# Kernel tuning notes

Measured on AMD Instinct MI355X. Metric: run time of the kernel, lower is better.

## Reference

```python
import jax, jax.numpy as jnp
import numpy as np

B, N, C, H = 2, 2048, 512, 8
D = C // H  # head dim = 64
SCALE = C ** -0.5  # module uses heads_channels**-0.5 (full inner dim, not per-head)


def setup_inputs() -> dict:
    key = jax.random.key(0)
    ks = jax.random.split(key, 9)
    return {
        "q": jax.random.normal(ks[0], (B, N, C), jnp.float32),
        "kv": jax.random.normal(ks[1], (B, N, C), jnp.float32),
        "pos_q": jax.random.normal(ks[2], (B, N, D), jnp.float32),
        "pos_k": jax.random.normal(ks[3], (B, N, D), jnp.float32),
        "Wq": jax.random.normal(ks[4], (C, C), jnp.float32) * (C ** -0.5),
        "Wk": jax.random.normal(ks[5], (C, C), jnp.float32) * (C ** -0.5),
        "Wv": jax.random.normal(ks[6], (C, C), jnp.float32) * (C ** -0.5),
        "Wo": jax.random.normal(ks[7], (C, C), jnp.float32) * (C ** -0.5),
        "bo": jnp.zeros((C,), jnp.float32),
    }


def reference(q, kv, pos_q, pos_k, Wq, Wk, Wv, Wo, bo):
    # projections: [b n c] @ [c c] -> [b n c]
    qp = q @ Wq
    kp = kv @ Wk
    vp = kv @ Wv
    # split heads: b n (h d) -> b h n d
    split = lambda t: t.reshape(B, N, H, D).transpose(0, 2, 1, 3)
    qh, kh, vh = split(qp), split(kp), split(vp)
    # additive positional bias, broadcast over heads: b n d -> b 1 n d
    qh = qh + pos_q[:, None, :, :]
    kh = kh + pos_k[:, None, :, :]
    sim = jnp.einsum("bhid,bhjd->bhij", qh, kh) * SCALE
    attn = jax.nn.softmax(sim, axis=-1)
    out = jnp.einsum("bhij,bhjd->bhid", attn, vh)
    # merge heads: b h n d -> b n (h d)
    out = out.transpose(0, 2, 1, 3).reshape(B, N, C)
    return out @ Wo + bo
```

## Files before the change

### kernel.cpp

```cpp
#include <hip/hip_runtime.h>
#include <hip/hip_bf16.h>
#include <stdint.h>
#include <math.h>

static constexpr int kB = 2, kN = 2048, kC = 512, kH = 8, kD = 64;
static constexpr float kScaleL2E =
    (float)(0.044194173824159216 * 1.4426950408889634);
static constexpr float kShift = 12.0f;
static constexpr int kSplit = 2;
static constexpr size_t kSegF = (size_t)kB * kN * kC;

typedef short bf16x8 __attribute__((ext_vector_type(8)));
typedef short bf16x4 __attribute__((ext_vector_type(4)));
typedef float f32x4  __attribute__((ext_vector_type(4)));

__device__ __forceinline__ float bf2f(unsigned short u) {
  union { unsigned int i; float f; } v; v.i = ((unsigned int)u) << 16; return v.f;
}
__device__ __forceinline__ unsigned short f2bf(float f) {
  union { float f; unsigned int i; } v; v.f = f;
  unsigned int x = v.i;
  return (unsigned short)((x + 0x7FFFu + ((x >> 16) & 1u)) >> 16);
}
__device__ __forceinline__ short f2bs(float f) { return (short)f2bf(f); }
__device__ __forceinline__ unsigned int pack2_t(float lo, float hi) {
  union { float f; unsigned int i; } a, b; a.f = lo; b.f = hi;
  return (b.i & 0xFFFF0000u) | (a.i >> 16);
}

__device__ __forceinline__ int vcol(int k) {
  return 32 * (k >> 5) + ((k >> 2) & 3) * 8 + ((k >> 4) & 1) * 4;
}

__global__ __launch_bounds__(256) void prep_kernel(
    const float* __restrict__ q, const float* __restrict__ kv,
    const float* __restrict__ Wq, const float* __restrict__ Wk,
    const float* __restrict__ Wv,
    unsigned short* __restrict__ qbf, unsigned short* __restrict__ kvbf,
    unsigned short* __restrict__ wT)
{
  const int t = threadIdx.x;
  if (blockIdx.z == 0) {
    const int gid = blockIdx.x * 256 + t;
    #pragma unroll
    for (int it = 0; it < 8; ++it) {
      int i4 = gid + it * 65536;
      float4 a = *(const float4*)(q + (size_t)i4 * 4);
      float4 b = *(const float4*)(kv + (size_t)i4 * 4);
      bf16x4 ab = {f2bs(a.x), f2bs(a.y), f2bs(a.z), f2bs(a.w)};
      bf16x4 bb = {f2bs(b.x), f2bs(b.y), f2bs(b.z), f2bs(b.w)};
      *(bf16x4*)(qbf + (size_t)i4 * 4) = ab;
      *(bf16x4*)(kvbf + (size_t)i4 * 4) = bb;
    }
  } else {
    if (blockIdx.x >= 192) return;
    const int wsel = blockIdx.x >> 6;
    const int tile = blockIdx.x & 63;
    const int tr = tile >> 3, tc = tile & 7;
    const float* W = (wsel == 0) ? Wq : (wsel == 1 ? Wk : Wv);
    unsigned short* out = wT + (size_t)wsel * kC * kC;

    __shared__ __align__(16) float Ts[64][68];
    #pragma unroll
    for (int it = 0; it < 4; ++it) {
      int e = t + it * 256;
      int r = e >> 4, c4 = (e & 15) * 4;
      *(float4*)&Ts[r][c4] =
          *(const float4*)(W + (size_t)(tr * 64 + r) * kC + tc * 64 + c4);
    }
    __syncthreads();
    const int n = t >> 2, ks = (t & 3) * 16;
    unsigned short* orow = out + (size_t)(tc * 64 + n) * kC + tr * 64 + ks;
    #pragma unroll
    for (int c = 0; c < 4; ++c) {
      ushort4 o;
      o.x = f2bf(Ts[ks + c * 4 + 0][n]);
      o.y = f2bf(Ts[ks + c * 4 + 1][n]);
      o.z = f2bf(Ts[ks + c * 4 + 2][n]);
      o.w = f2bf(Ts[ks + c * 4 + 3][n]);
      *(ushort4*)(orow + c * 4) = o;
    }
  }
}

__global__ __launch_bounds__(256) void proj_kernel(
    const unsigned short* __restrict__ qbf,
    const unsigned short* __restrict__ kvbf,
    const unsigned short* __restrict__ wT,
    const float* __restrict__ pos_q,
    const float* __restrict__ pos_k,
    unsigned short* __restrict__ qh,
    unsigned short* __restrict__ kh,
    unsigned short* __restrict__ vhT)
{
  const bool kvmode = (blockIdx.z == 1);
  const unsigned short* A = kvmode ? kvbf : qbf;
  const unsigned short* Bt0 = wT + (kvmode ? (size_t)kC * kC : 0);
  const unsigned short* Bt1 = wT + 2 * (size_t)kC * kC;

  __shared__ __align__(16) unsigned short As[128][72];
  __shared__ __align__(16) unsigned short Bs[2][64][72];

  const int t = threadIdx.x;
  const int w = t >> 6, lane = t & 63;
  const int l15 = lane & 15, quad = lane >> 4;
  const int m0 = blockIdx.x * 128;
  const int n0 = blockIdx.y * 64;

  const int sr = t >> 3, sc = (t & 7) * 8;

  bf16x8 pa[4], pb0[2], pb1[2];
  #pragma unroll
  for (int i = 0; i < 4; ++i)
    pa[i] = *(const bf16x8*)(A + (size_t)(m0 + sr + i * 32) * kC + sc);
  #pragma unroll
  for (int i = 0; i < 2; ++i)
    pb0[i] = *(const bf16x8*)(Bt0 + (size_t)(n0 + sr + i * 32) * kC + sc);
  if (kvmode)
    #pragma unroll
    for (int i = 0; i < 2; ++i)
      pb1[i] = *(const bf16x8*)(Bt1 + (size_t)(n0 + sr + i * 32) * kC + sc);

  f32x4 acc0[2][4], acc1[2][4];
  #pragma unroll
  for (int si = 0; si < 2; ++si)
    #pragma unroll
    for (int ct = 0; ct < 4; ++ct) {
      acc0[si][ct] = (f32x4){0.f, 0.f, 0.f, 0.f};
      acc1[si][ct] = (f32x4){0.f, 0.f, 0.f, 0.f};
    }

  for (int k0 = 0; k0 < kC; k0 += 64) {
    if (k0) __syncthreads();
    #pragma unroll
    for (int i = 0; i < 4; ++i) *(bf16x8*)&As[sr + i * 32][sc] = pa[i];
    #pragma unroll
    for (int i = 0; i < 2; ++i) *(bf16x8*)&Bs[0][sr + i * 32][sc] = pb0[i];
    if (kvmode)
      #pragma unroll
      for (int i = 0; i < 2; ++i) *(bf16x8*)&Bs[1][sr + i * 32][sc] = pb1[i];
    __syncthreads();
    if (k0 + 64 < kC) {
      int kn = k0 + 64;
      #pragma unroll
      for (int i = 0; i < 4; ++i)
        pa[i] = *(const bf16x8*)(A + (size_t)(m0 + sr + i * 32) * kC + kn + sc);
      #pragma unroll
      for (int i = 0; i < 2; ++i)
        pb0[i] = *(const bf16x8*)(Bt0 + (size_t)(n0 + sr + i * 32) * kC + kn + sc);
      if (kvmode)
        #pragma unroll
        for (int i = 0; i < 2; ++i)
          pb1[i] = *(const bf16x8*)(Bt1 + (size_t)(n0 + sr + i * 32) * kC + kn + sc);
    }
    bf16x8 a0[2], a1[2];
    #pragma unroll
    for (int si = 0; si < 2; ++si) {
      a0[si] = *(const bf16x8*)&As[w * 32 + si * 16 + l15][quad * 8];
      a1[si] = *(const bf16x8*)&As[w * 32 + si * 16 + l15][32 + quad * 8];
    }
    #pragma unroll
    for (int ct = 0; ct < 4; ++ct) {
      bf16x8 b0 = *(const bf16x8*)&Bs[0][ct * 16 + l15][quad * 8];
      bf16x8 b1 = *(const bf16x8*)&Bs[0][ct * 16 + l15][32 + quad * 8];
      #pragma unroll
      for (int si = 0; si < 2; ++si) {
        acc0[si][ct] = __builtin_amdgcn_mfma_f32_16x16x32_bf16(a0[si], b0, acc0[si][ct], 0, 0, 0);
        acc0[si][ct] = __builtin_amdgcn_mfma_f32_16x16x32_bf16(a1[si], b1, acc0[si][ct], 0, 0, 0);
      }
      if (kvmode) {
        bf16x8 c0 = *(const bf16x8*)&Bs[1][ct * 16 + l15][quad * 8];
        bf16x8 c1 = *(const bf16x8*)&Bs[1][ct * 16 + l15][32 + quad * 8];
        #pragma unroll
        for (int si = 0; si < 2; ++si) {
          acc1[si][ct] = __builtin_amdgcn_mfma_f32_16x16x32_bf16(a0[si], c0, acc1[si][ct], 0, 0, 0);
          acc1[si][ct] = __builtin_amdgcn_mfma_f32_16x16x32_bf16(a1[si], c1, acc1[si][ct], 0, 0, 0);
        }
      }
    }
  }

  const int h = n0 >> 6;
  if (!kvmode) {
    #pragma unroll
    for (int si = 0; si < 2; ++si)
      #pragma unroll
      for (int r = 0; r < 4; ++r) {
        int m = m0 + w * 32 + si * 16 + quad * 4 + r;
        int b = m >> 11, n_seq = m & (kN - 1);
        #pragma unroll
        for (int ct = 0; ct < 4; ++ct) {
          int d = ct * 16 + l15;
          float val = (acc0[si][ct][r] +
                       pos_q[((size_t)b * kN + n_seq) * kD + d]) * kScaleL2E;
          qh[(((size_t)b * kH + h) * kN + n_seq) * kD + d] = f2bf(val);
        }
      }
  } else {
    #pragma unroll
    for (int si = 0; si < 2; ++si)
      #pragma unroll
      for (int r = 0; r < 4; ++r) {
        int m = m0 + w * 32 + si * 16 + quad * 4 + r;
        int b = m >> 11, n_seq = m & (kN - 1);
        #pragma unroll
        for (int ct = 0; ct < 4; ++ct) {
          int d = ct * 16 + l15;
          float vk = acc0[si][ct][r] + pos_k[((size_t)b * kN + n_seq) * kD + d];
          kh[(((size_t)b * kH + h) * kN + n_seq) * kD + d] = f2bf(vk);
        }
      }
    __syncthreads();
    unsigned short (*Tv)[136] = (unsigned short(*)[136])&As[0][0];
    #pragma unroll
    for (int si = 0; si < 2; ++si)
      #pragma unroll
      for (int ct = 0; ct < 4; ++ct) {
        const int d = ct * 16 + l15;
        const int nl = w * 32 + si * 16 + quad * 4;
        unsigned int lo = (unsigned int)f2bf(acc1[si][ct][0]) |
                          ((unsigned int)f2bf(acc1[si][ct][1]) << 16);
        unsigned int hi = (unsigned int)f2bf(acc1[si][ct][2]) |
                          ((unsigned int)f2bf(acc1[si][ct][3]) << 16);
        *(unsigned int*)&Tv[d][nl]     = lo;
        *(unsigned int*)&Tv[d][nl + 2] = hi;
      }
    __syncthreads();
    const int c16 = t & 15, dr = t >> 4;
    const int b2 = m0 >> 11, nbase = m0 & (kN - 1);
    #pragma unroll
    for (int rep = 0; rep < 4; ++rep) {
      const int d = rep * 16 + dr;
      bf16x8 vv = *(const bf16x8*)&Tv[d][c16 * 8];
      *(bf16x8*)(vhT + (((size_t)(b2 * kH + h)) * kD + d) * kN + nbase + c16 * 8) = vv;
    }
  }
}

__global__ __launch_bounds__(256, 8) void attn_kernel(
    const unsigned short* __restrict__ qh,
    const unsigned short* __restrict__ kh,
    const unsigned short* __restrict__ vhT,
    unsigned short* __restrict__ opart,
    float* __restrict__ lbuf)
{
  const int sid = (blockIdx.x & 7) * 128 + (blockIdx.x >> 3);
  const int s  = sid >> 9;
  const int bh = (sid >> 5) & 15;
  const int q0 = (sid & 31) * 64;
  const int b = bh >> 3, h = bh & 7;
  const int kbase = s * (kN / kSplit);
  const int nkt = kN / kSplit / 64;
  const int t = threadIdx.x;
  const int w = t >> 6, lane = t & 63;
  const int l15 = lane & 15, quad = lane >> 4;

  __shared__ __align__(16) unsigned short Kb_s[64][72];
  __shared__ __align__(16) unsigned short Vt_s[64][72];

  const unsigned short* Qb = qh  + (size_t)bh * kN * kD;
  const unsigned short* Kb = kh  + (size_t)bh * kN * kD;
  const unsigned short* Vb = vhT + (size_t)bh * kD * kN;

  bf16x8 aq0, aq1;
  {
    const unsigned short* qrow = Qb + (size_t)(q0 + w * 16 + l15) * kD;
    aq0 = *(const bf16x8*)(qrow + quad * 8);
    aq1 = *(const bf16x8*)(qrow + 32 + quad * 8);
  }

  const int sr = t >> 3, sc = (t & 7) * 8, sr2 = sr + 32;
  const int vc1 = vcol(sc), vc2 = vcol(sc + 4);

  bf16x8 pk0 = *(const bf16x8*)(Kb + (size_t)(kbase + sr) * kD + sc);
  bf16x8 pk1 = *(const bf16x8*)(Kb + (size_t)(kbase + sr2) * kD + sc);
  bf16x8 pv0 = *(const bf16x8*)(Vb + (size_t)sr * kN + kbase + sc);
  bf16x8 pv1 = *(const bf16x8*)(Vb + (size_t)sr2 * kN + kbase + sc);

  f32x4 o[4];
  #pragma unroll
  for (int nt = 0; nt < 4; ++nt) o[nt] = (f32x4){0.f, 0.f, 0.f, 0.f};
  float l_run = 0.f;

  for (int i = 0; i < nkt; ++i) {
    __syncthreads();
    *(bf16x8*)&Kb_s[sr][sc]  = pk0;
    *(bf16x8*)&Kb_s[sr2][sc] = pk1;
    {
      bf16x4 lo0 = {pv0[0], pv0[1], pv0[2], pv0[3]};
      bf16x4 hi0 = {pv0[4], pv0[5], pv0[6], pv0[7]};
      bf16x4 lo1 = {pv1[0], pv1[1], pv1[2], pv1[3]};
      bf16x4 hi1 = {pv1[4], pv1[5], pv1[6], pv1[7]};
      *(bf16x4*)&Vt_s[sr][vc1]  = lo0;
      *(bf16x4*)&Vt_s[sr][vc2]  = hi0;
      *(bf16x4*)&Vt_s[sr2][vc1] = lo1;
      *(bf16x4*)&Vt_s[sr2][vc2] = hi1;
    }
    __syncthreads();

    f32x4 sacc[4];
    __builtin_amdgcn_s_setprio(1);
    #pragma unroll
    for (int ct = 0; ct < 4; ++ct) {
      bf16x8 ak0 = *(const bf16x8*)&Kb_s[ct * 16 + l15][quad * 8];
      bf16x8 ak1 = *(const bf16x8*)&Kb_s[ct * 16 + l15][32 + quad * 8];
      f32x4 zz = (f32x4){0.f, 0.f, 0.f, 0.f};
      zz = __builtin_amdgcn_mfma_f32_16x16x32_bf16(ak0, aq0, zz, 0, 0, 0);
      zz = __builtin_amdgcn_mfma_f32_16x16x32_bf16(ak1, aq1, zz, 0, 0, 0);
      sacc[ct] = zz;
    }
    __builtin_amdgcn_s_setprio(0);

    if (i + 1 < nkt) {
      int ktn = kbase + (i + 1) * 64;
      pk0 = *(const bf16x8*)(Kb + (size_t)(ktn + sr) * kD + sc);
      pk1 = *(const bf16x8*)(Kb + (size_t)(ktn + sr2) * kD + sc);
    }

    union PB8 { unsigned int u[4]; bf16x8 v; } pb01, pb23;
    {
      float psum = 0.f;
      #pragma unroll
      for (int ct = 0; ct < 4; ++ct)
        #pragma unroll
        for (int r = 0; r < 4; ++r) {
          float p = exp2f(sacc[ct][r] - kShift);
          sacc[ct][r] = p;
          psum += p;
        }
      l_run += psum;
      pb01.u[0] = pack2_t(sacc[0][0], sacc[0][1]);
      pb01.u[1] = pack2_t(sacc[0][2], sacc[0][3]);
      pb01.u[2] = pack2_t(sacc[1][0], sacc[1][1]);
      pb01.u[3] = pack2_t(sacc[1][2], sacc[1][3]);
      pb23.u[0] = pack2_t(sacc[2][0], sacc[2][1]);
      pb23.u[1] = pack2_t(sacc[2][2], sacc[2][3]);
      pb23.u[2] = pack2_t(sacc[3][0], sacc[3][1]);
      pb23.u[3] = pack2_t(sacc[3][2], sacc[3][3]);
    }

    if (i + 1 < nkt) {
      int ktn = kbase + (i + 1) * 64;
      pv0 = *(const bf16x8*)(Vb + (size_t)sr * kN + ktn + sc);
      pv1 = *(const bf16x8*)(Vb + (size_t)sr2 * kN + ktn + sc);
    }

    __builtin_amdgcn_s_setprio(1);
    #pragma unroll
    for (int nt = 0; nt < 4; ++nt) {
      bf16x8 av0 = *(const bf16x8*)&Vt_s[nt * 16 + l15][quad * 8];
      bf16x8 av1 = *(const bf16x8*)&Vt_s[nt * 16 + l15][32 + quad * 8];
      o[nt] = __builtin_amdgcn_mfma_f32_16x16x32_bf16(av0, pb01.v, o[nt], 0, 0, 0);
      o[nt] = __builtin_amdgcn_mfma_f32_16x16x32_bf16(av1, pb23.v, o[nt], 0, 0, 0);
    }
    __builtin_amdgcn_s_setprio(0);
  }

  l_run += __shfl_xor(l_run, 16);
  l_run += __shfl_xor(l_run, 32);
  if (quad == 0)
    lbuf[(size_t)(s * 16 + bh) * kN + q0 + w * 16 + l15] = l_run;

  __syncthreads();
  unsigned short (*Ot)[72] = (unsigned short(*)[72])&Kb_s[0][0];
  {
    const int ql = w * 16 + l15;
    #pragma unroll
    for (int nt = 0; nt < 4; ++nt) {
      unsigned int lo = (unsigned int)f2bf(o[nt][0]) |
                        ((unsigned int)f2bf(o[nt][1]) << 16);
      unsigned int hi = (unsigned int)f2bf(o[nt][2]) |
                        ((unsigned int)f2bf(o[nt][3]) << 16);
      const int d0 = nt * 16 + quad * 4;
      *(unsigned int*)&Ot[ql][d0]     = lo;
      *(unsigned int*)&Ot[ql][d0 + 2] = hi;
    }
  }
  __syncthreads();
  {
    unsigned short* od = opart + (size_t)s * kSegF;
    const int c8 = t & 7, qb = t >> 3;
    #pragma unroll
    for (int rep = 0; rep < 2; ++rep) {
      const int ql = rep * 32 + qb;
      bf16x8 vv = *(const bf16x8*)&Ot[ql][c8 * 8];
      *(bf16x8*)(od + ((size_t)b * kN + (q0 + ql)) * kC + h * kD + c8 * 8) = vv;
    }
  }
}

__global__ __launch_bounds__(256) void proj_out_kernel(
    const unsigned short* __restrict__ opart,
    const float* __restrict__ lbuf,
    const float* __restrict__ Wo,
    const float* __restrict__ bo,
    float* __restrict__ out)
{
  __shared__ __align__(16) unsigned short Wt[64][72];

  const int t = threadIdx.x;
  const int w = t >> 6, lane = t & 63;
  const int l15 = lane & 15, quad = lane >> 4;
  const int m0 = blockIdx.x * 64;
  const int n0 = blockIdx.y * 64;

  const int m = m0 + w * 16 + l15;
  const int nseq = m & (kN - 1);
  const int bb = m >> 11;
  const size_t arow = (size_t)m * kC;

  ushort4 pw[4];
  #pragma unroll
  for (int i = 0; i < 4; ++i) {
    int e = t + i * 256;
    int r = e >> 4, c4 = (e & 15) * 4;
    float4 wv = *(const float4*)(Wo + (size_t)r * kC + n0 + c4);
    pw[i] = make_ushort4(f2bf(wv.x), f2bf(wv.y), f2bf(wv.z), f2bf(wv.w));
  }

  f32x4 acc[4];
  #pragma unroll
  for (int ct = 0; ct < 4; ++ct) acc[ct] = (f32x4){0.f, 0.f, 0.f, 0.f};

  #pragma unroll
  for (int k0 = 0; k0 < kC; k0 += 64) {
    if (k0) __syncthreads();
    #pragma unroll
    for (int i = 0; i < 4; ++i) {
      int e = t + i * 256;
      int r = e >> 4, c4 = (e & 15) * 4;
      Wt[c4 + 0][r] = pw[i].x;
      Wt[c4 + 1][r] = pw[i].y;
      Wt[c4 + 2][r] = pw[i].z;
      Wt[c4 + 3][r] = pw[i].w;
    }
    __syncthreads();

    const int h = k0 >> 6;
    const int bh = bb * 8 + h;
    float lsum = 0.f;
    #pragma unroll
    for (int s = 0; s < kSplit; ++s)
      lsum += lbuf[(size_t)(s * 16 + bh) * kN + nseq];
    const float wgt = 1.f / lsum;

    float af0[8] = {}, af1[8] = {};
    #pragma unroll
    for (int s = 0; s < kSplit; ++s) {
      bf16x8 v0 = *(const bf16x8*)(opart + (size_t)s * kSegF + arow + k0 + quad * 8);
      bf16x8 v1 = *(const bf16x8*)(opart + (size_t)s * kSegF + arow + k0 + 32 + quad * 8);
      #pragma unroll
      for (int j = 0; j < 8; ++j) {
        af0[j] += bf2f((unsigned short)v0[j]);
        af1[j] += bf2f((unsigned short)v1[j]);
      }
    }
    bf16x8 a0, a1;
    #pragma unroll
    for (int j = 0; j < 8; ++j) {
      a0[j] = (short)f2bf(af0[j] * wgt);
      a1[j] = (short)f2bf(af1[j] * wgt);
    }

    if (k0 + 64 < kC) {
      int kn = k0 + 64;
      #pragma unroll
      for (int i = 0; i < 4; ++i) {
        int e = t + i * 256;
        int r = e >> 4, c4 = (e & 15) * 4;
        float4 wv = *(const float4*)(Wo + (size_t)(kn + r) * kC + n0 + c4);
        pw[i] = make_ushort4(f2bf(wv.x), f2bf(wv.y), f2bf(wv.z), f2bf(wv.w));
      }
    }
    #pragma unroll
    for (int ct = 0; ct < 4; ++ct) {
      bf16x8 b0 = *(const bf16x8*)&Wt[ct * 16 + l15][quad * 8];
      bf16x8 b1 = *(const bf16x8*)&Wt[ct * 16 + l15][32 + quad * 8];
      acc[ct] = __builtin_amdgcn_mfma_f32_16x16x32_bf16(a0, b0, acc[ct], 0, 0, 0);
      acc[ct] = __builtin_amdgcn_mfma_f32_16x16x32_bf16(a1, b1, acc[ct], 0, 0, 0);
    }
  }

  #pragma unroll
  for (int ct = 0; ct < 4; ++ct) {
    int n = n0 + ct * 16 + l15;
    float bb2 = bo[n];
    #pragma unroll
    for (int r = 0; r < 4; ++r) {
      int mm = m0 + w * 16 + quad * 4 + r;
      out[(size_t)mm * kC + n] = acc[ct][r] + bb2;
    }
  }
}

extern "C" void kernel_launch(void* const* d_in, const int* in_sizes, int n_in,
                              void* d_out, int out_size, void* d_ws, size_t ws_size,
                              hipStream_t stream) {
  (void)in_sizes; (void)n_in; (void)out_size; (void)ws_size;
  const float* q     = (const float*)d_in[0];
  const float* kv    = (const float*)d_in[1];
  const float* pos_q = (const float*)d_in[2];
  const float* pos_k = (const float*)d_in[3];
  const float* Wq    = (const float*)d_in[4];
  const float* Wk    = (const float*)d_in[5];
  const float* Wv    = (const float*)d_in[6];
  const float* Wo    = (const float*)d_in[7];
  const float* bo    = (const float*)d_in[8];
  float* out = (float*)d_out;

  const size_t seg = (size_t)kB * kH * kN * kD;

  unsigned short* qbf  = (unsigned short*)d_ws;
  unsigned short* kvbf = qbf + seg;
  unsigned short* wT   = kvbf + seg;
  unsigned short* qhp  = wT + 3 * (size_t)kC * kC;
  unsigned short* khp  = qhp + seg;
  unsigned short* vtp  = khp + seg;
  unsigned short* opart = vtp + seg;
  float* lbuf = (float*)(opart + (size_t)kSplit * kSegF);

  dim3 blk(256);
  prep_kernel<<<dim3(256, 1, 2), blk, 0, stream>>>(q, kv, Wq, Wk, Wv, qbf, kvbf, wT);
  proj_kernel<<<dim3(32, 8, 2), blk, 0, stream>>>(qbf, kvbf, wT, pos_q, pos_k,
                                                  qhp, khp, vtp);
  attn_kernel<<<dim3(1024), blk, 0, stream>>>(qhp, khp, vtp, opart, lbuf);
  proj_out_kernel<<<dim3(64, 8), blk, 0, stream>>>(opart, lbuf, Wo, bo, out);
}
```

Baseline: 149.0 us.

## Pretranspose Wo in prep kernel and halve proj_kernel M-tile for more blocks

The prep kernel now also converts Wo to transposed bf16 using its previously idle blocks 192-255. The output projection then reads bf16 fragments of Wo straight from global memory, with no per-block fp32 load, conversion, LDS transpose or syncs. Separately, the projection kernel's M tile drops from 128 to 64 rows, doubling the grid to raise occupancy and parallelism, at the cost of less reuse of the weight tiles.

```diff
diff --git a/kernel.cpp b/kernel.cpp
--- a/kernel.cpp
+++ b/kernel.cpp
@@ -35,7 +35,7 @@
 __global__ __launch_bounds__(256) void prep_kernel(
     const float* __restrict__ q, const float* __restrict__ kv,
     const float* __restrict__ Wq, const float* __restrict__ Wk,
-    const float* __restrict__ Wv,
+    const float* __restrict__ Wv, const float* __restrict__ Wo,
     unsigned short* __restrict__ qbf, unsigned short* __restrict__ kvbf,
     unsigned short* __restrict__ wT)
 {
@@ -53,11 +53,10 @@
       *(bf16x4*)(kvbf + (size_t)i4 * 4) = bb;
     }
   } else {
-    if (blockIdx.x >= 192) return;
     const int wsel = blockIdx.x >> 6;
     const int tile = blockIdx.x & 63;
     const int tr = tile >> 3, tc = tile & 7;
-    const float* W = (wsel == 0) ? Wq : (wsel == 1 ? Wk : Wv);
+    const float* W = (wsel == 0) ? Wq : (wsel == 1 ? Wk : (wsel == 2 ? Wv : Wo));
     unsigned short* out = wT + (size_t)wsel * kC * kC;
 
     __shared__ __align__(16) float Ts[64][68];
@@ -98,20 +97,20 @@
   const unsigned short* Bt0 = wT + (kvmode ? (size_t)kC * kC : 0);
   const unsigned short* Bt1 = wT + 2 * (size_t)kC * kC;
 
-  __shared__ __align__(16) unsigned short As[128][72];
+  __shared__ __align__(16) unsigned short As[64][72];
   __shared__ __align__(16) unsigned short Bs[2][64][72];
 
   const int t = threadIdx.x;
   const int w = t >> 6, lane = t & 63;
   const int l15 = lane & 15, quad = lane >> 4;
-  const int m0 = blockIdx.x * 128;
+  const int m0 = blockIdx.x * 64;
   const int n0 = blockIdx.y * 64;
 
   const int sr = t >> 3, sc = (t & 7) * 8;
 
-  bf16x8 pa[4], pb0[2], pb1[2];
-  #pragma unroll
-  for (int i = 0; i < 4; ++i)
+  bf16x8 pa[2], pb0[2], pb1[2];
+  #pragma unroll
+  for (int i = 0; i < 2; ++i)
     pa[i] = *(const bf16x8*)(A + (size_t)(m0 + sr + i * 32) * kC + sc);
   #pragma unroll
   for (int i = 0; i < 2; ++i)
@@ -121,19 +120,17 @@
     for (int i = 0; i < 2; ++i)
       pb1[i] = *(const bf16x8*)(Bt1 + (size_t)(n0 + sr + i * 32) * kC + sc);
 
-  f32x4 acc0[2][4], acc1[2][4];
-  #pragma unroll
-  for (int si = 0; si < 2; ++si)
-    #pragma unroll
-    for (int ct = 0; ct < 4; ++ct) {
-      acc0[si][ct] = (f32x4){0.f, 0.f, 0.f, 0.f};
-      acc1[si][ct] = (f32x4){0.f, 0.f, 0.f, 0.f};
-    }
+  f32x4 acc0[4], acc1[4];
+  #pragma unroll
+  for (int ct = 0; ct < 4; ++ct) {
+    acc0[ct] = (f32x4){0.f, 0.f, 0.f, 0.f};
+    acc1[ct] = (f32x4){0.f, 0.f, 0.f, 0.f};
+  }
 
   for (int k0 = 0; k0 < kC; k0 += 64) {
     if (k0) __syncthreads();
     #pragma unroll
-    for (int i = 0; i < 4; ++i) *(bf16x8*)&As[sr + i * 32][sc] = pa[i];
+    for (int i = 0; i < 2; ++i) *(bf16x8*)&As[sr + i * 32][sc] = pa[i];
     #pragma unroll
     for (int i = 0; i < 2; ++i) *(bf16x8*)&Bs[0][sr + i * 32][sc] = pb0[i];
     if (kvmode)
@@ -143,7 +140,7 @@
     if (k0 + 64 < kC) {
       int kn = k0 + 64;
       #pragma unroll
-      for (int i = 0; i < 4; ++i)
+      for (int i = 0; i < 2; ++i)
         pa[i] = *(const bf16x8*)(A + (size_t)(m0 + sr + i * 32) * kC + kn + sc);
       #pragma unroll
       for (int i = 0; i < 2; ++i)
@@ -153,29 +150,19 @@
         for (int i = 0; i < 2; ++i)
           pb1[i] = *(const bf16x8*)(Bt1 + (size_t)(n0 + sr + i * 32) * kC + kn + sc);
     }
-    bf16x8 a0[2], a1[2];
-    #pragma unroll
-    for (int si = 0; si < 2; ++si) {
-      a0[si] = *(const bf16x8*)&As[w * 32 + si * 16 + l15][quad * 8];
-      a1[si] = *(const bf16x8*)&As[w * 32 + si * 16 + l15][32 + quad * 8];
-    }
+    bf16x8 a0 = *(const bf16x8*)&As[w * 16 + l15][quad * 8];
+    bf16x8 a1 = *(const bf16x8*)&As[w * 16 + l15][32 + quad * 8];
     #pragma unroll
     for (int ct = 0; ct < 4; ++ct) {
       bf16x8 b0 = *(const bf16x8*)&Bs[0][ct * 16 + l15][quad * 8];
       bf16x8 b1 = *(const bf16x8*)&Bs[0][ct * 16 + l15][32 + quad * 8];
-      #pragma unroll
-      for (int si = 0; si < 2; ++si) {
-        acc0[si][ct] = __builtin_amdgcn_mfma_f32_16x16x32_bf16(a0[si], b0, acc0[si][ct], 0, 0, 0);
-        acc0[si][ct] = __builtin_amdgcn_mfma_f32_16x16x32_bf16(a1[si], b1, acc0[si][ct], 0, 0, 0);
-      }
+      acc0[ct] = __builtin_amdgcn_mfma_f32_16x16x32_bf16(a0, b0, acc0[ct], 0, 0, 0);
+      acc0[ct] = __builtin_amdgcn_mfma_f32_16x16x32_bf16(a1, b1, acc0[ct], 0, 0, 0);
       if (kvmode) {
         bf16x8 c0 = *(const bf16x8*)&Bs[1][ct * 16 + l15][quad * 8];
         bf16x8 c1 = *(const bf16x8*)&Bs[1][ct * 16 + l15][32 + quad * 8];
-        #pragma unroll
-        for (int si = 0; si < 2; ++si) {
-          acc1[si][ct] = __builtin_amdgcn_mfma_f32_16x16x32_bf16(a0[si], c0, acc1[si][ct], 0, 0, 0);
-          acc1[si][ct] = __builtin_amdgcn_mfma_f32_16x16x32_bf16(a1[si], c1, acc1[si][ct], 0, 0, 0);
-        }
+        acc1[ct] = __builtin_amdgcn_mfma_f32_16x16x32_bf16(a0, c0, acc1[ct], 0, 0, 0);
+        acc1[ct] = __builtin_amdgcn_mfma_f32_16x16x32_bf16(a1, c1, acc1[ct], 0, 0, 0);
       }
     }
   }
@@ -183,56 +170,50 @@
   const int h = n0 >> 6;
   if (!kvmode) {
     #pragma unroll
-    for (int si = 0; si < 2; ++si)
-      #pragma unroll
-      for (int r = 0; r < 4; ++r) {
-        int m = m0 + w * 32 + si * 16 + quad * 4 + r;
-        int b = m >> 11, n_seq = m & (kN - 1);
-        #pragma unroll
-        for (int ct = 0; ct < 4; ++ct) {
-          int d = ct * 16 + l15;
-          float val = (acc0[si][ct][r] +
-                       pos_q[((size_t)b * kN + n_seq) * kD + d]) * kScaleL2E;
-          qh[(((size_t)b * kH + h) * kN + n_seq) * kD + d] = f2bf(val);
-        }
+    for (int r = 0; r < 4; ++r) {
+      int m = m0 + w * 16 + quad * 4 + r;
+      int b = m >> 11, n_seq = m & (kN - 1);
+      #pragma unroll
+      for (int ct = 0; ct < 4; ++ct) {
+        int d = ct * 16 + l15;
+        float val = (acc0[ct][r] +
+                     pos_q[((size_t)b * kN + n_seq) * kD + d]) * kScaleL2E;
+        qh[(((size_t)b * kH + h) * kN + n_seq) * kD + d] = f2bf(val);
       }
+    }
   } else {
     #pragma unroll
-    for (int si = 0; si < 2; ++si)
-      #pragma unroll
-      for (int r = 0; r < 4; ++r) {
-        int m = m0 + w * 32 + si * 16 + quad * 4 + r;
-        int b = m >> 11, n_seq = m & (kN - 1);
-        #pragma unroll
-        for (int ct = 0; ct < 4; ++ct) {
-          int d = ct * 16 + l15;
-          float vk = acc0[si][ct][r] + pos_k[((size_t)b * kN + n_seq) * kD + d];
-          kh[(((size_t)b * kH + h) * kN + n_seq) * kD + d] = f2bf(vk);
-        }
+    for (int r = 0; r < 4; ++r) {
+      int m = m0 + w * 16 + quad * 4 + r;
+      int b = m >> 11, n_seq = m & (kN - 1);
+      #pragma unroll
+      for (int ct = 0; ct < 4; ++ct) {
+        int d = ct * 16 + l15;
+        float vk = acc0[ct][r] + pos_k[((size_t)b * kN + n_seq) * kD + d];
+        kh[(((size_t)b * kH + h) * kN + n_seq) * kD + d] = f2bf(vk);
       }
-    __syncthreads();
-    unsigned short (*Tv)[136] = (unsigned short(*)[136])&As[0][0];
-    #pragma unroll
-    for (int si = 0; si < 2; ++si)
-      #pragma unroll
-      for (int ct = 0; ct < 4; ++ct) {
-        const int d = ct * 16 + l15;
-        const int nl = w * 32 + si * 16 + quad * 4;
-        unsigned int lo = (unsigned int)f2bf(acc1[si][ct][0]) |
-                          ((unsigned int)f2bf(acc1[si][ct][1]) << 16);
-        unsigned int hi = (unsigned int)f2bf(acc1[si][ct][2]) |
-                          ((unsigned int)f2bf(acc1[si][ct][3]) << 16);
-        *(unsigned int*)&Tv[d][nl]     = lo;
-        *(unsigned int*)&Tv[d][nl + 2] = hi;
-      }
-    __syncthreads();
-    const int c16 = t & 15, dr = t >> 4;
+    }
+    __syncthreads();
+    unsigned short (*Tv)[72] = (unsigned short(*)[72])&As[0][0];
+    #pragma unroll
+    for (int ct = 0; ct < 4; ++ct) {
+      const int d = ct * 16 + l15;
+      const int nl = w * 16 + quad * 4;
+      unsigned int lo = (unsigned int)f2bf(acc1[ct][0]) |
+                        ((unsigned int)f2bf(acc1[ct][1]) << 16);
+      unsigned int hi = (unsigned int)f2bf(acc1[ct][2]) |
+                        ((unsigned int)f2bf(acc1[ct][3]) << 16);
+      *(unsigned int*)&Tv[d][nl]     = lo;
+      *(unsigned int*)&Tv[d][nl + 2] = hi;
+    }
+    __syncthreads();
+    const int c8 = t & 7, dr = t >> 3;
     const int b2 = m0 >> 11, nbase = m0 & (kN - 1);
     #pragma unroll
-    for (int rep = 0; rep < 4; ++rep) {
-      const int d = rep * 16 + dr;
-      bf16x8 vv = *(const bf16x8*)&Tv[d][c16 * 8];
-      *(bf16x8*)(vhT + (((size_t)(b2 * kH + h)) * kD + d) * kN + nbase + c16 * 8) = vv;
+    for (int rep = 0; rep < 2; ++rep) {
+      const int d = rep * 32 + dr;
+      bf16x8 vv = *(const bf16x8*)&Tv[d][c8 * 8];
+      *(bf16x8*)(vhT + (((size_t)(b2 * kH + h)) * kD + d) * kN + nbase + c8 * 8) = vv;
     }
   }
 }
@@ -392,12 +373,10 @@
 __global__ __launch_bounds__(256) void proj_out_kernel(
     const unsigned short* __restrict__ opart,
     const float* __restrict__ lbuf,
-    const float* __restrict__ Wo,
+    const unsigned short* __restrict__ WoT,
     const float* __restrict__ bo,
     float* __restrict__ out)
 {
-  __shared__ __align__(16) unsigned short Wt[64][72];
-
   const int t = threadIdx.x;
   const int w = t >> 6, lane = t & 63;
   const int l15 = lane & 15, quad = lane >> 4;
@@ -409,33 +388,12 @@
   const int bb = m >> 11;
   const size_t arow = (size_t)m * kC;
 
-  ushort4 pw[4];
-  #pragma unroll
-  for (int i = 0; i < 4; ++i) {
-    int e = t + i * 256;
-    int r = e >> 4, c4 = (e & 15) * 4;
-    float4 wv = *(const float4*)(Wo + (size_t)r * kC + n0 + c4);
-    pw[i] = make_ushort4(f2bf(wv.x), f2bf(wv.y), f2bf(wv.z), f2bf(wv.w));
-  }
-
   f32x4 acc[4];
   #pragma unroll
   for (int ct = 0; ct < 4; ++ct) acc[ct] = (f32x4){0.f, 0.f, 0.f, 0.f};
 
   #pragma unroll
   for (int k0 = 0; k0 < kC; k0 += 64) {
-    if (k0) __syncthreads();
-    #pragma unroll
-    for (int i = 0; i < 4; ++i) {
-      int e = t + i * 256;
-      int r = e >> 4, c4 = (e & 15) * 4;
-      Wt[c4 + 0][r] = pw[i].x;
-      Wt[c4 + 1][r] = pw[i].y;
-      Wt[c4 + 2][r] = pw[i].z;
-      Wt[c4 + 3][r] = pw[i].w;
-    }
-    __syncthreads();
-
     const int h = k0 >> 6;
     const int bh = bb * 8 + h;
     float lsum = 0.f;
@@ -462,20 +420,11 @@
       a1[j] = (short)f2bf(af1[j] * wgt);
     }
 
-    if (k0 + 64 < kC) {
-      int kn = k0 + 64;
-      #pragma unroll
-      for (int i = 0; i < 4; ++i) {
-        int e = t + i * 256;
-        int r = e >> 4, c4 = (e & 15) * 4;
-        float4 wv = *(const float4*)(Wo + (size_t)(kn + r) * kC + n0 + c4);
-        pw[i] = make_ushort4(f2bf(wv.x), f2bf(wv.y), f2bf(wv.z), f2bf(wv.w));
-      }
-    }
     #pragma unroll
     for (int ct = 0; ct < 4; ++ct) {
-      bf16x8 b0 = *(const bf16x8*)&Wt[ct * 16 + l15][quad * 8];
-      bf16x8 b1 = *(const bf16x8*)&Wt[ct * 16 + l15][32 + quad * 8];
+      const unsigned short* wrow = WoT + (size_t)(n0 + ct * 16 + l15) * kC + k0;
+      bf16x8 b0 = *(const bf16x8*)(wrow + quad * 8);
+      bf16x8 b1 = *(const bf16x8*)(wrow + 32 + quad * 8);
       acc[ct] = __builtin_amdgcn_mfma_f32_16x16x32_bf16(a0, b0, acc[ct], 0, 0, 0);
       acc[ct] = __builtin_amdgcn_mfma_f32_16x16x32_bf16(a1, b1, acc[ct], 0, 0, 0);
     }
@@ -513,16 +462,19 @@
   unsigned short* qbf  = (unsigned short*)d_ws;
   unsigned short* kvbf = qbf + seg;
   unsigned short* wT   = kvbf + seg;
-  unsigned short* qhp  = wT + 3 * (size_t)kC * kC;
+  unsigned short* qhp  = wT + 4 * (size_t)kC * kC;
   unsigned short* khp  = qhp + seg;
   unsigned short* vtp  = khp + seg;
   unsigned short* opart = vtp + seg;
   float* lbuf = (float*)(opart + (size_t)kSplit * kSegF);
 
   dim3 blk(256);
-  prep_kernel<<<dim3(256, 1, 2), blk, 0, stream>>>(q, kv, Wq, Wk, Wv, qbf, kvbf, wT);
-  proj_kernel<<<dim3(32, 8, 2), blk, 0, stream>>>(qbf, kvbf, wT, pos_q, pos_k,
+  prep_kernel<<<dim3(256, 1, 2), blk, 0, stream>>>(q, kv, Wq, Wk, Wv, Wo,
+                                                   qbf, kvbf, wT);
+  proj_kernel<<<dim3(64, 8, 2), blk, 0, stream>>>(qbf, kvbf, wT, pos_q, pos_k,
                                                   qhp, khp, vtp);
   attn_kernel<<<dim3(1024), blk, 0, stream>>>(qhp, khp, vtp, opart, lbuf);
-  proj_out_kernel<<<dim3(64, 8), blk, 0, stream>>>(opart, lbuf, Wo, bo, out);
-}
+  proj_out_kernel<<<dim3(64, 8), blk, 0, stream>>>(opart, lbuf,
+                                                   wT + 3 * (size_t)kC * kC,
+                                                   bo, out);
+}
```

Result: slower. 166.3 us (+11.6%).
